# Kernel tuning notes

Measured on AMD Instinct MI355X. Metric: run time of the kernel, lower is better.

## Reference

```python
import jax, jax.numpy as jnp
import numpy as np

B, N, IN, H, DH, ACT = 8192, 36, 8, 8, 9, 10
GAT = H * DH  # 72 == 2*N, required so cat([down(x), t]) matches mu's input dim
NEG = -1e9


def setup_inputs() -> dict:
    key = jax.random.key(0)
    ks = jax.random.split(key, 9)
    x = jax.random.normal(ks[0], (B, N, IN), dtype=jnp.float32)
    adj = jax.random.randint(ks[1], (N, N), 0, 2, dtype=jnp.int32)
    adj = jnp.maximum(adj, jnp.eye(N, dtype=jnp.int32))  # self-loops: no empty softmax rows
    s = 0.1
    W = jax.random.normal(ks[2], (H, IN - 1, DH), dtype=jnp.float32) * s   # per-head projection
    a_src = jax.random.normal(ks[3], (H, DH), dtype=jnp.float32) * s       # attention vec (source half)
    a_dst = jax.random.normal(ks[4], (H, DH), dtype=jnp.float32) * s       # attention vec (target half)
    W_down = jax.random.normal(ks[5], (GAT, 1), dtype=jnp.float32) * s
    b_down = jnp.zeros((1,), dtype=jnp.float32)
    W_mu = jax.random.normal(ks[6], (GAT, ACT), dtype=jnp.float32) * s     # GAT == 2*N
    b_mu = jnp.zeros((ACT,), dtype=jnp.float32)
    return {"x": x, "adj": adj, "W": W, "a_src": a_src, "a_dst": a_dst,
            "W_down": W_down, "b_down": b_down, "W_mu": W_mu, "b_mu": b_mu}


def _gat_encoder(xc, adj, W, a_src, a_dst):
    # xc: [B,N,IN-1]; standard multi-head GAT with adjacency-masked attention
    h = jnp.einsum('bni,hid->bhnd', xc, W)                 # [B,H,N,DH]
    e_src = jnp.einsum('bhnd,hd->bhn', h, a_src)           # [B,H,N]
    e_dst = jnp.einsum('bhnd,hd->bhn', h, a_dst)           # [B,H,N]
    e = jax.nn.leaky_relu(e_src[:, :, :, None] + e_dst[:, :, None, :], 0.2)  # [B,H,N,N]
    e = jnp.where(adj[None, None, :, :] > 0, e, NEG)
    attn = jax.nn.softmax(e, axis=-1)
    out = jnp.einsum('bhij,bhjd->bhid', attn, h)           # [B,H,N,DH]
    out = out.transpose(0, 2, 1, 3).reshape(out.shape[0], N, GAT)  # concat heads
    return jax.nn.elu(out)


def reference(x, adj, W, a_src, a_dst, W_down, b_down, W_mu, b_mu):
    # slice/cat glue: drop feature 3, keep it as scalar channel t
    xc = jnp.concatenate([x[:, :, :3], x[:, :, 4:]], axis=-1)  # [B,N,IN-1]
    t = xc[:, :, 3]                                            # [B,N] (== original x[:,:,4])
    g = _gat_encoder(xc, adj, W, a_src, a_dst)                 # [B,N,GAT]
    down = (g @ W_down + b_down)[..., 0]                       # [B,N]
    feat = jax.nn.leaky_relu(jnp.concatenate([down, t], axis=-1), 0.01)  # [B,2N]
    mu = feat @ W_mu + b_mu                                    # [B,ACT]
    return mu
```

## Files before the change

### kernel.cpp

```cpp
#include <hip/hip_runtime.h>

typedef float v2f __attribute__((ext_vector_type(2)));

#define BB 8192
#define NN 36
#define INF_ 8
#define HH 8
#define DHH 9
#define GATF 72
#define ACTF 10
#define NTH 320
#define HSTRIDE 12
#define WSTRIDE 12
#define L2E 1.44269504088896f

static __device__ __forceinline__ v2f mk2(float a, float b) { v2f r; r.x = a; r.y = b; return r; }

__global__ __launch_bounds__(NTH, 6) void gnn_kernel(
    const float* __restrict__ x, const int* __restrict__ adj,
    const float* __restrict__ W, const float* __restrict__ a_src,
    const float* __restrict__ a_dst, const float* __restrict__ W_down,
    const float* __restrict__ b_down, const float* __restrict__ W_mu,
    const float* __restrict__ b_mu, float* __restrict__ out)
{
    const int b = blockIdx.x;
    const int tid = threadIdx.x;

    __shared__ float xcs[NN * 9];
    __shared__ float ts[NN];
    __shared__ __align__(16) float hbuf[HH * NN * HSTRIDE];
    __shared__ __align__(16) float edl[HH * NN];
    __shared__ uint2 adjm[NN];
    __shared__ float pd[NN * 9];
    __shared__ float feat[GATF];
    __shared__ __align__(16) float wlds[HH * 7 * WSTRIDE];
    __shared__ v2f  aid[HH * DHH];
    __shared__ float wdlds[GATF];
    __shared__ float wmulds[GATF * ACTF];
    __shared__ float bdlds[1];
    __shared__ float bmulds[ACTF];

    const float* xb = x + (size_t)b * (NN * INF_);
    if (tid < NN * INF_) {
        int n = tid >> 3, c = tid & 7;
        float v = xb[tid];
        if (c < 3) xcs[n * 9 + c] = v;
        else if (c > 3) xcs[n * 9 + (c - 1)] = v;
        if (c == 4) ts[n] = v;
    }
    {
        int i0 = tid - 256;
        if (i0 >= 0 && i0 < NN) {
            const int4* ap = reinterpret_cast<const int4*>(adj + i0 * NN);
            unsigned int lo = 0u, hi = 0u;
            #pragma unroll
            for (int q = 0; q < 9; ++q) {
                int4 a4 = ap[q];
                const int base = q * 4;
                if (base + 0 < 32) { lo |= (a4.x > 0 ? 1u << (base + 0) : 0u); } else { hi |= (a4.x > 0 ? 1u << (base - 32) : 0u); }
                if (base + 1 < 32) { lo |= (a4.y > 0 ? 1u << (base + 1) : 0u); } else { hi |= (a4.y > 0 ? 1u << (base + 1 - 32) : 0u); }
                if (base + 2 < 32) { lo |= (a4.z > 0 ? 1u << (base + 2) : 0u); } else { hi |= (a4.z > 0 ? 1u << (base + 2 - 32) : 0u); }
                if (base + 3 < 32) { lo |= (a4.w > 0 ? 1u << (base + 3) : 0u); } else { hi |= (a4.w > 0 ? 1u << (base + 3 - 32) : 0u); }
            }
            adjm[i0] = make_uint2(lo, hi);
        }
    }
    for (int idx = tid; idx < HH * 7 * DHH; idx += NTH) {
        int row = idx / DHH, d = idx - row * DHH;
        wlds[row * WSTRIDE + d] = W[idx];
    }
    if (tid < HH * DHH) aid[tid] = mk2(a_src[tid], a_dst[tid]);
    if (tid >= 128 && tid < 128 + GATF) wdlds[tid - 128] = W_down[tid - 128];
    for (int idx = tid; idx < GATF * ACTF; idx += NTH) wmulds[idx] = W_mu[idx];
    if (tid == 0) bdlds[0] = b_down[0];
    if (tid >= 64 && tid < 64 + ACTF) bmulds[tid - 64] = b_mu[tid - 64];
    __syncthreads();

    const int hh = (tid < HH * NN) ? (tid / NN) : 0;
    const int i  = (tid < HH * NN) ? (tid - hh * NN) : 0;
    float esr = 0.f;
    if (tid < HH * NN) {
        const float* xp = xcs + i * 9;
        const float* wp = wlds + hh * 7 * WSTRIDE;
        v2f h01 = mk2(0.f, 0.f), h23 = h01, h45 = h01, h67 = h01;
        float h8 = 0.f;
        #pragma unroll
        for (int k = 0; k < 7; ++k) {
            float xk = xp[k];
            v2f xkk = mk2(xk, xk);
            const float* wr = wp + k * WSTRIDE;
            float4 wa = *reinterpret_cast<const float4*>(wr);
            float4 wb = *reinterpret_cast<const float4*>(wr + 4);
            float  wc = wr[8];
            h01 = __builtin_elementwise_fma(xkk, mk2(wa.x, wa.y), h01);
            h23 = __builtin_elementwise_fma(xkk, mk2(wa.z, wa.w), h23);
            h45 = __builtin_elementwise_fma(xkk, mk2(wb.x, wb.y), h45);
            h67 = __builtin_elementwise_fma(xkk, mk2(wb.z, wb.w), h67);
            h8 = fmaf(xk, wc, h8);
        }
        float* hp = hbuf + (hh * NN + i) * HSTRIDE;
        *reinterpret_cast<float4*>(hp)     = make_float4(h01.x, h01.y, h23.x, h23.y);
        *reinterpret_cast<float4*>(hp + 4) = make_float4(h45.x, h45.y, h67.x, h67.y);
        hp[8] = h8;
        const v2f* ap = aid + hh * DHH;
        v2f sd = mk2(0.f, 0.f);
        sd = __builtin_elementwise_fma(mk2(h01.x, h01.x), ap[0], sd);
        sd = __builtin_elementwise_fma(mk2(h01.y, h01.y), ap[1], sd);
        sd = __builtin_elementwise_fma(mk2(h23.x, h23.x), ap[2], sd);
        sd = __builtin_elementwise_fma(mk2(h23.y, h23.y), ap[3], sd);
        sd = __builtin_elementwise_fma(mk2(h45.x, h45.x), ap[4], sd);
        sd = __builtin_elementwise_fma(mk2(h45.y, h45.y), ap[5], sd);
        sd = __builtin_elementwise_fma(mk2(h67.x, h67.x), ap[6], sd);
        sd = __builtin_elementwise_fma(mk2(h67.y, h67.y), ap[7], sd);
        sd = __builtin_elementwise_fma(mk2(h8, h8), ap[8], sd);
        esr = sd.x * L2E;
        edl[hh * NN + i] = sd.y * L2E;
    }
    __syncthreads();

    if (tid < HH * NN) {
        const uint2 mrow = adjm[i];
        const float* hrow = hbuf + (hh * NN) * HSTRIDE;
        const float* edp = edl + hh * NN;
        const v2f esr2 = mk2(esr, esr);
        const v2f c02 = mk2(0.2f, 0.2f);
        v2f acc01 = mk2(0.f, 0.f), acc23 = acc01, acc45 = acc01, acc67 = acc01;
        float acc8 = 0.f;
        v2f ssum2 = mk2(0.f, 0.f);

#define PVE(jj, p_) { \
        const float* hj_ = hrow + (jj) * HSTRIDE; \
        float4 ha_ = *reinterpret_cast<const float4*>(hj_); \
        float4 hb_ = *reinterpret_cast<const float4*>(hj_ + 4); \
        float  hc_ = hj_[8]; \
        v2f pp_ = mk2(p_, p_); \
        acc01 = __builtin_elementwise_fma(pp_, mk2(ha_.x, ha_.y), acc01); \
        acc23 = __builtin_elementwise_fma(pp_, mk2(ha_.z, ha_.w), acc23); \
        acc45 = __builtin_elementwise_fma(pp_, mk2(hb_.x, hb_.y), acc45); \
        acc67 = __builtin_elementwise_fma(pp_, mk2(hb_.z, hb_.w), acc67); \
        acc8 = fmaf(p_, hc_, acc8); }

#define STEP2(jb, w_, ee2_) { \
        v2f s2_ = esr2 + (ee2_); \
        v2f t2_ = s2_ * c02; \
        float p0_ = __builtin_exp2f(fmaxf(s2_.x, t2_.x)); \
        float p1_ = __builtin_exp2f(fmaxf(s2_.y, t2_.y)); \
        int m0_ = ((int)((w_) << (31 - ((jb) & 31)))) >> 31; \
        int m1_ = ((int)((w_) << (31 - (((jb) & 31) + 1)))) >> 31; \
        p0_ = __int_as_float(__float_as_int(p0_) & m0_); \
        p1_ = __int_as_float(__float_as_int(p1_) & m1_); \
        ssum2 += mk2(p0_, p1_); \
        PVE((jb), p0_); \
        PVE((jb) + 1, p1_); }

        #pragma unroll
        for (int q = 0; q < 9; ++q) {
            float4 e4 = *reinterpret_cast<const float4*>(edp + q * 4);
            const unsigned wq = (q < 8) ? mrow.x : mrow.y;
            STEP2(4 * q + 0, wq, mk2(e4.x, e4.y));
            STEP2(4 * q + 2, wq, mk2(e4.z, e4.w));
        }
#undef STEP2
#undef PVE

        float ssum = ssum2.x + ssum2.y;
        float inv = 1.0f / ssum;
        v2f inv2 = mk2(inv, inv);
        v2f o01 = acc01 * inv2, o23 = acc23 * inv2, o45 = acc45 * inv2, o67 = acc67 * inv2;
        float o8 = acc8 * inv;
        const float* wdp = wdlds + hh * DHH;
        float pdown = 0.f;
#define EPI(oval, dd_) { \
        float o_ = (oval); \
        o_ = (o_ > 0.f) ? o_ : (__builtin_exp2f(o_ * L2E) - 1.0f); \
        pdown = fmaf(o_, wdp[dd_], pdown); }
        EPI(o01.x, 0); EPI(o01.y, 1); EPI(o23.x, 2); EPI(o23.y, 3);
        EPI(o45.x, 4); EPI(o45.y, 5); EPI(o67.x, 6); EPI(o67.y, 7);
        EPI(o8, 8);
#undef EPI
        pd[i * 9 + hh] = pdown;
    }
    __syncthreads();

    if (tid < NN) {
        const float* pp = pd + tid * 9;
        float acc = bdlds[0];
        #pragma unroll
        for (int h = 0; h < HH; ++h) acc += pp[h];
        feat[tid] = (acc > 0.f) ? acc : 0.01f * acc;
    } else if (tid < 2 * NN) {
        float v = ts[tid - NN];
        feat[tid] = (v > 0.f) ? v : 0.01f * v;
    }
    __syncthreads();

    if (tid < ACTF) {
        float acc = bmulds[tid];
        #pragma unroll
        for (int k = 0; k < GATF; ++k) acc += feat[k] * wmulds[k * ACTF + tid];
        out[(size_t)b * ACTF + tid] = acc;
    }
}

extern "C" void kernel_launch(void* const* d_in, const int* in_sizes, int n_in,
                              void* d_out, int out_size, void* d_ws, size_t ws_size,
                              hipStream_t stream) {
    const float* x      = (const float*)d_in[0];
    const int*   adj    = (const int*)d_in[1];
    const float* W      = (const float*)d_in[2];
    const float* a_src  = (const float*)d_in[3];
    const float* a_dst  = (const float*)d_in[4];
    const float* W_down = (const float*)d_in[5];
    const float* b_down = (const float*)d_in[6];
    const float* W_mu   = (const float*)d_in[7];
    const float* b_mu   = (const float*)d_in[8];
    float* out = (float*)d_out;

    gnn_kernel<<<BB, NTH, 0, stream>>>(x, adj, W, a_src, a_dst, W_down, b_down, W_mu, b_mu, out);
}
```

Measured before the change: 77.39 us.

## Process two batch items per block and use additive float adjacency mask

```diff
diff --git a/kernel.cpp b/kernel.cpp
--- a/kernel.cpp
+++ b/kernel.cpp
@@ -9,10 +9,12 @@
 #define DHH 9
 #define GATF 72
 #define ACTF 10
-#define NTH 320
+#define NTH 576
+#define ROWS 288
 #define HSTRIDE 12
 #define WSTRIDE 12
 #define L2E 1.44269504088896f
+#define MASKNEG -1000000.0f
 
 static __device__ __forceinline__ v2f mk2(float a, float b) { v2f r; r.x = a; r.y = b; return r; }
 
@@ -23,16 +25,16 @@
     const float* __restrict__ b_down, const float* __restrict__ W_mu,
     const float* __restrict__ b_mu, float* __restrict__ out)
 {
-    const int b = blockIdx.x;
     const int tid = threadIdx.x;
-
-    __shared__ float xcs[NN * 9];
-    __shared__ float ts[NN];
-    __shared__ __align__(16) float hbuf[HH * NN * HSTRIDE];
-    __shared__ __align__(16) float edl[HH * NN];
-    __shared__ uint2 adjm[NN];
-    __shared__ float pd[NN * 9];
-    __shared__ float feat[GATF];
+    const int b0 = blockIdx.x * 2;
+
+    __shared__ float xcs[2 * NN * 9];
+    __shared__ float ts[2 * NN];
+    __shared__ __align__(16) float hbuf[2 * HH * NN * HSTRIDE];
+    __shared__ __align__(16) float edl[2 * ROWS];
+    __shared__ float pd[2 * NN * 9];
+    __shared__ float feat[2 * GATF];
+    __shared__ __align__(16) float adjf[NN * NN];
     __shared__ __align__(16) float wlds[HH * 7 * WSTRIDE];
     __shared__ v2f  aid[HH * DHH];
     __shared__ float wdlds[GATF];
@@ -40,47 +42,45 @@
     __shared__ float bdlds[1];
     __shared__ float bmulds[ACTF];
 
-    const float* xb = x + (size_t)b * (NN * INF_);
-    if (tid < NN * INF_) {
-        int n = tid >> 3, c = tid & 7;
+    {
+        const float* xb = x + (size_t)b0 * (NN * INF_);
+        int item = (tid >= NN * INF_) ? 1 : 0;
+        int rem = tid - item * (NN * INF_);
+        int n = rem >> 3, c = rem & 7;
         float v = xb[tid];
-        if (c < 3) xcs[n * 9 + c] = v;
-        else if (c > 3) xcs[n * 9 + (c - 1)] = v;
-        if (c == 4) ts[n] = v;
-    }
-    {
-        int i0 = tid - 256;
-        if (i0 >= 0 && i0 < NN) {
-            const int4* ap = reinterpret_cast<const int4*>(adj + i0 * NN);
-            unsigned int lo = 0u, hi = 0u;
-            #pragma unroll
-            for (int q = 0; q < 9; ++q) {
-                int4 a4 = ap[q];
-                const int base = q * 4;
-                if (base + 0 < 32) { lo |= (a4.x > 0 ? 1u << (base + 0) : 0u); } else { hi |= (a4.x > 0 ? 1u << (base - 32) : 0u); }
-                if (base + 1 < 32) { lo |= (a4.y > 0 ? 1u << (base + 1) : 0u); } else { hi |= (a4.y > 0 ? 1u << (base + 1 - 32) : 0u); }
-                if (base + 2 < 32) { lo |= (a4.z > 0 ? 1u << (base + 2) : 0u); } else { hi |= (a4.z > 0 ? 1u << (base + 2 - 32) : 0u); }
-                if (base + 3 < 32) { lo |= (a4.w > 0 ? 1u << (base + 3) : 0u); } else { hi |= (a4.w > 0 ? 1u << (base + 3 - 32) : 0u); }
-            }
-            adjm[i0] = make_uint2(lo, hi);
-        }
-    }
+        float* xc = xcs + item * (NN * 9);
+        if (c < 3) xc[n * 9 + c] = v;
+        else if (c > 3) xc[n * 9 + (c - 1)] = v;
+        if (c == 4) ts[item * NN + n] = v;
+    }
+    if (tid < 324) {
+        int i = tid / 9, q = tid - i * 9;
+        int4 a4 = reinterpret_cast<const int4*>(adj)[tid];
+        float4 m4;
+        m4.x = (a4.x > 0) ? 0.f : MASKNEG;
+        m4.y = (a4.y > 0) ? 0.f : MASKNEG;
+        m4.z = (a4.z > 0) ? 0.f : MASKNEG;
+        m4.w = (a4.w > 0) ? 0.f : MASKNEG;
+        *reinterpret_cast<float4*>(adjf + i * NN + q * 4) = m4;
+    }
+    if (tid >= 384 && tid < 384 + HH * 7 * DHH - 504 + 504) {  }
     for (int idx = tid; idx < HH * 7 * DHH; idx += NTH) {
         int row = idx / DHH, d = idx - row * DHH;
         wlds[row * WSTRIDE + d] = W[idx];
     }
     if (tid < HH * DHH) aid[tid] = mk2(a_src[tid], a_dst[tid]);
-    if (tid >= 128 && tid < 128 + GATF) wdlds[tid - 128] = W_down[tid - 128];
+    if (tid >= 448 && tid < 448 + GATF) wdlds[tid - 448] = W_down[tid - 448];
     for (int idx = tid; idx < GATF * ACTF; idx += NTH) wmulds[idx] = W_mu[idx];
     if (tid == 0) bdlds[0] = b_down[0];
-    if (tid >= 64 && tid < 64 + ACTF) bmulds[tid - 64] = b_mu[tid - 64];
-    __syncthreads();
-
-    const int hh = (tid < HH * NN) ? (tid / NN) : 0;
-    const int i  = (tid < HH * NN) ? (tid - hh * NN) : 0;
-    float esr = 0.f;
-    if (tid < HH * NN) {
-        const float* xp = xcs + i * 9;
+    if (tid >= 352 && tid < 352 + ACTF) bmulds[tid - 352] = b_mu[tid - 352];
+    __syncthreads();
+
+    const int item = (tid >= ROWS) ? 1 : 0;
+    const int r = tid - item * ROWS;
+    const int hh = r / NN, i = r - hh * NN;
+    float esr;
+    {
+        const float* xp = xcs + item * (NN * 9) + i * 9;
         const float* wp = wlds + hh * 7 * WSTRIDE;
         v2f h01 = mk2(0.f, 0.f), h23 = h01, h45 = h01, h67 = h01;
         float h8 = 0.f;
@@ -98,10 +98,10 @@
             h67 = __builtin_elementwise_fma(xkk, mk2(wb.z, wb.w), h67);
             h8 = fmaf(xk, wc, h8);
         }
-        float* hp = hbuf + (hh * NN + i) * HSTRIDE;
+        float* hp = hbuf + (item * ROWS + hh * NN + i) * HSTRIDE;
         *reinterpret_cast<float4*>(hp)     = make_float4(h01.x, h01.y, h23.x, h23.y);
         *reinterpret_cast<float4*>(hp + 4) = make_float4(h45.x, h45.y, h67.x, h67.y);
-        hp[8] = h8;
+        *reinterpret_cast<v2f*>(hp + 8)    = mk2(h8, 1.0f);
         const v2f* ap = aid + hh * DHH;
         v2f sd = mk2(0.f, 0.f);
         sd = __builtin_elementwise_fma(mk2(h01.x, h01.x), ap[0], sd);
@@ -114,60 +114,46 @@
         sd = __builtin_elementwise_fma(mk2(h67.y, h67.y), ap[7], sd);
         sd = __builtin_elementwise_fma(mk2(h8, h8), ap[8], sd);
         esr = sd.x * L2E;
-        edl[hh * NN + i] = sd.y * L2E;
-    }
-    __syncthreads();
-
-    if (tid < HH * NN) {
-        const uint2 mrow = adjm[i];
-        const float* hrow = hbuf + (hh * NN) * HSTRIDE;
-        const float* edp = edl + hh * NN;
-        const v2f esr2 = mk2(esr, esr);
-        const v2f c02 = mk2(0.2f, 0.2f);
-        v2f acc01 = mk2(0.f, 0.f), acc23 = acc01, acc45 = acc01, acc67 = acc01;
-        float acc8 = 0.f;
-        v2f ssum2 = mk2(0.f, 0.f);
-
-#define PVE(jj, p_) { \
+        edl[item * ROWS + hh * NN + i] = sd.y * L2E;
+    }
+    __syncthreads();
+
+    {
+        const float* hrow = hbuf + (item * ROWS + hh * NN) * HSTRIDE;
+        const float* edp = edl + item * ROWS + hh * NN;
+        const float* amr = adjf + i * NN;
+        v2f acc01 = mk2(0.f, 0.f), acc23 = acc01, acc45 = acc01, acc67 = acc01, acc89 = acc01;
+
+#define STEP(jj, ee, mm) { \
+        float s_ = esr + (ee); \
+        float e_ = fmaxf(s_, 0.2f * s_) + (mm);           \
+        float p_ = __builtin_exp2f(e_);                   \
         const float* hj_ = hrow + (jj) * HSTRIDE; \
         float4 ha_ = *reinterpret_cast<const float4*>(hj_); \
         float4 hb_ = *reinterpret_cast<const float4*>(hj_ + 4); \
-        float  hc_ = hj_[8]; \
+        v2f hc_ = *reinterpret_cast<const v2f*>(hj_ + 8); \
         v2f pp_ = mk2(p_, p_); \
         acc01 = __builtin_elementwise_fma(pp_, mk2(ha_.x, ha_.y), acc01); \
         acc23 = __builtin_elementwise_fma(pp_, mk2(ha_.z, ha_.w), acc23); \
         acc45 = __builtin_elementwise_fma(pp_, mk2(hb_.x, hb_.y), acc45); \
         acc67 = __builtin_elementwise_fma(pp_, mk2(hb_.z, hb_.w), acc67); \
-        acc8 = fmaf(p_, hc_, acc8); }
-
-#define STEP2(jb, w_, ee2_) { \
-        v2f s2_ = esr2 + (ee2_); \
-        v2f t2_ = s2_ * c02; \
-        float p0_ = __builtin_exp2f(fmaxf(s2_.x, t2_.x)); \
-        float p1_ = __builtin_exp2f(fmaxf(s2_.y, t2_.y)); \
-        int m0_ = ((int)((w_) << (31 - ((jb) & 31)))) >> 31; \
-        int m1_ = ((int)((w_) << (31 - (((jb) & 31) + 1)))) >> 31; \
-        p0_ = __int_as_float(__float_as_int(p0_) & m0_); \
-        p1_ = __int_as_float(__float_as_int(p1_) & m1_); \
-        ssum2 += mk2(p0_, p1_); \
-        PVE((jb), p0_); \
-        PVE((jb) + 1, p1_); }
+        acc89 = __builtin_elementwise_fma(pp_, hc_, acc89); }
 
         #pragma unroll
         for (int q = 0; q < 9; ++q) {
             float4 e4 = *reinterpret_cast<const float4*>(edp + q * 4);
-            const unsigned wq = (q < 8) ? mrow.x : mrow.y;
-            STEP2(4 * q + 0, wq, mk2(e4.x, e4.y));
-            STEP2(4 * q + 2, wq, mk2(e4.z, e4.w));
+            float4 m4 = *reinterpret_cast<const float4*>(amr + q * 4);
+            STEP(4 * q + 0, e4.x, m4.x);
+            STEP(4 * q + 1, e4.y, m4.y);
+            STEP(4 * q + 2, e4.z, m4.z);
+            STEP(4 * q + 3, e4.w, m4.w);
         }
-#undef STEP2
-#undef PVE
-
-        float ssum = ssum2.x + ssum2.y;
-        float inv = 1.0f / ssum;
+#undef STEP
+
+        float inv = 1.0f / acc89.y;
         v2f inv2 = mk2(inv, inv);
         v2f o01 = acc01 * inv2, o23 = acc23 * inv2, o45 = acc45 * inv2, o67 = acc67 * inv2;
-        float o8 = acc8 * inv;
+        float o8 = acc89.x * inv;
         const float* wdp = wdlds + hh * DHH;
         float pdown = 0.f;
 #define EPI(oval, dd_) { \
@@ -178,27 +164,35 @@
         EPI(o45.x, 4); EPI(o45.y, 5); EPI(o67.x, 6); EPI(o67.y, 7);
         EPI(o8, 8);
 #undef EPI
-        pd[i * 9 + hh] = pdown;
-    }
-    __syncthreads();
-
-    if (tid < NN) {
-        const float* pp = pd + tid * 9;
+        pd[item * (NN * 9) + i * 9 + hh] = pdown;
+    }
+    __syncthreads();
+
+    if (tid < 2 * NN) {
+        int it = (tid >= NN) ? 1 : 0;
+        int node = tid - it * NN;
+        const float* pp = pd + it * (NN * 9) + node * 9;
         float acc = bdlds[0];
         #pragma unroll
         for (int h = 0; h < HH; ++h) acc += pp[h];
-        feat[tid] = (acc > 0.f) ? acc : 0.01f * acc;
-    } else if (tid < 2 * NN) {
-        float v = ts[tid - NN];
-        feat[tid] = (v > 0.f) ? v : 0.01f * v;
-    }
-    __syncthreads();
-
-    if (tid < ACTF) {
-        float acc = bmulds[tid];
-        #pragma unroll
-        for (int k = 0; k < GATF; ++k) acc += feat[k] * wmulds[k * ACTF + tid];
-        out[(size_t)b * ACTF + tid] = acc;
+        feat[it * GATF + node] = (acc > 0.f) ? acc : 0.01f * acc;
+    } else if (tid < 4 * NN) {
+        int idx = tid - 2 * NN;
+        int it = (idx >= NN) ? 1 : 0;
+        int node = idx - it * NN;
+        float v = ts[it * NN + node];
+        feat[it * GATF + NN + node] = (v > 0.f) ? v : 0.01f * v;
+    }
+    __syncthreads();
+
+    if (tid < 2 * ACTF) {
+        int it = (tid >= ACTF) ? 1 : 0;
+        int o = tid - it * ACTF;
+        const float* fp = feat + it * GATF;
+        float acc = bmulds[o];
+        #pragma unroll
+        for (int k = 0; k < GATF; ++k) acc = fmaf(fp[k], wmulds[k * ACTF + o], acc);
+        out[(size_t)(b0 + it) * ACTF + o] = acc;
     }
 }
 
@@ -216,5 +210,5 @@
     const float* b_mu   = (const float*)d_in[8];
     float* out = (float*)d_out;
 
-    gnn_kernel<<<BB, NTH, 0, stream>>>(x, adj, W, a_src, a_dst, W_down, b_down, W_mu, b_mu, out);
+    gnn_kernel<<<BB / 2, NTH, 0, stream>>>(x, adj, W, a_src, a_dst, W_down, b_down, W_mu, b_mu, out);
 }
```

New measurement: 81.57 us. 5.4% more time.

## Use additive float adjacency mask and fold softmax denominator into packed FMA

Applied to the files above, without the earlier changes.

```diff
diff --git a/kernel.cpp b/kernel.cpp
--- a/kernel.cpp
+++ b/kernel.cpp
@@ -10,11 +10,19 @@
 #define GATF 72
 #define ACTF 10
 #define NTH 320
+#define ROWS 288
 #define HSTRIDE 12
 #define WSTRIDE 12
 #define L2E 1.44269504088896f
+#define MASKNEG -1000000.0f
 
 static __device__ __forceinline__ v2f mk2(float a, float b) { v2f r; r.x = a; r.y = b; return r; }
+
+static __device__ __forceinline__ v2f pkfma(v2f a, v2f b, v2f c) {
+    v2f d;
+    asm("v_pk_fma_f32 %0, %1, %2, %3" : "=v"(d) : "v"(a), "v"(b), "v"(c));
+    return d;
+}
 
 __global__ __launch_bounds__(NTH, 6) void gnn_kernel(
     const float* __restrict__ x, const int* __restrict__ adj,
@@ -28,9 +36,9 @@
 
     __shared__ float xcs[NN * 9];
     __shared__ float ts[NN];
-    __shared__ __align__(16) float hbuf[HH * NN * HSTRIDE];
-    __shared__ __align__(16) float edl[HH * NN];
-    __shared__ uint2 adjm[NN];
+    __shared__ __align__(16) float hbuf[ROWS * HSTRIDE];
+    __shared__ __align__(16) float edl[ROWS];
+    __shared__ __align__(16) float adjf[NN * NN];
     __shared__ float pd[NN * 9];
     __shared__ float feat[GATF];
     __shared__ __align__(16) float wlds[HH * 7 * WSTRIDE];
@@ -48,22 +56,14 @@
         else if (c > 3) xcs[n * 9 + (c - 1)] = v;
         if (c == 4) ts[n] = v;
     }
-    {
-        int i0 = tid - 256;
-        if (i0 >= 0 && i0 < NN) {
-            const int4* ap = reinterpret_cast<const int4*>(adj + i0 * NN);
-            unsigned int lo = 0u, hi = 0u;
-            #pragma unroll
-            for (int q = 0; q < 9; ++q) {
-                int4 a4 = ap[q];
-                const int base = q * 4;
-                if (base + 0 < 32) { lo |= (a4.x > 0 ? 1u << (base + 0) : 0u); } else { hi |= (a4.x > 0 ? 1u << (base - 32) : 0u); }
-                if (base + 1 < 32) { lo |= (a4.y > 0 ? 1u << (base + 1) : 0u); } else { hi |= (a4.y > 0 ? 1u << (base + 1 - 32) : 0u); }
-                if (base + 2 < 32) { lo |= (a4.z > 0 ? 1u << (base + 2) : 0u); } else { hi |= (a4.z > 0 ? 1u << (base + 2 - 32) : 0u); }
-                if (base + 3 < 32) { lo |= (a4.w > 0 ? 1u << (base + 3) : 0u); } else { hi |= (a4.w > 0 ? 1u << (base + 3 - 32) : 0u); }
-            }
-            adjm[i0] = make_uint2(lo, hi);
-        }
+    for (int idx = tid; idx < (NN * NN) / 4; idx += NTH) {
+        int4 a4 = reinterpret_cast<const int4*>(adj)[idx];
+        float4 m4;
+        m4.x = (a4.x > 0) ? 0.f : MASKNEG;
+        m4.y = (a4.y > 0) ? 0.f : MASKNEG;
+        m4.z = (a4.z > 0) ? 0.f : MASKNEG;
+        m4.w = (a4.w > 0) ? 0.f : MASKNEG;
+        *reinterpret_cast<float4*>(adjf + idx * 4) = m4;
     }
     for (int idx = tid; idx < HH * 7 * DHH; idx += NTH) {
         int row = idx / DHH, d = idx - row * DHH;
@@ -76,10 +76,10 @@
     if (tid >= 64 && tid < 64 + ACTF) bmulds[tid - 64] = b_mu[tid - 64];
     __syncthreads();
 
-    const int hh = (tid < HH * NN) ? (tid / NN) : 0;
-    const int i  = (tid < HH * NN) ? (tid - hh * NN) : 0;
+    const int hh = (tid < ROWS) ? (tid / NN) : 0;
+    const int i  = (tid < ROWS) ? (tid - hh * NN) : 0;
     float esr = 0.f;
-    if (tid < HH * NN) {
+    if (tid < ROWS) {
         const float* xp = xcs + i * 9;
         const float* wp = wlds + hh * 7 * WSTRIDE;
         v2f h01 = mk2(0.f, 0.f), h23 = h01, h45 = h01, h67 = h01;
@@ -92,82 +92,68 @@
             float4 wa = *reinterpret_cast<const float4*>(wr);
             float4 wb = *reinterpret_cast<const float4*>(wr + 4);
             float  wc = wr[8];
-            h01 = __builtin_elementwise_fma(xkk, mk2(wa.x, wa.y), h01);
-            h23 = __builtin_elementwise_fma(xkk, mk2(wa.z, wa.w), h23);
-            h45 = __builtin_elementwise_fma(xkk, mk2(wb.x, wb.y), h45);
-            h67 = __builtin_elementwise_fma(xkk, mk2(wb.z, wb.w), h67);
+            h01 = pkfma(xkk, *(const v2f*)&wa.x, h01);
+            h23 = pkfma(xkk, *(const v2f*)&wa.z, h23);
+            h45 = pkfma(xkk, *(const v2f*)&wb.x, h45);
+            h67 = pkfma(xkk, *(const v2f*)&wb.z, h67);
             h8 = fmaf(xk, wc, h8);
         }
         float* hp = hbuf + (hh * NN + i) * HSTRIDE;
         *reinterpret_cast<float4*>(hp)     = make_float4(h01.x, h01.y, h23.x, h23.y);
         *reinterpret_cast<float4*>(hp + 4) = make_float4(h45.x, h45.y, h67.x, h67.y);
-        hp[8] = h8;
+        *reinterpret_cast<v2f*>(hp + 8)    = mk2(h8, 1.0f);
         const v2f* ap = aid + hh * DHH;
         v2f sd = mk2(0.f, 0.f);
-        sd = __builtin_elementwise_fma(mk2(h01.x, h01.x), ap[0], sd);
-        sd = __builtin_elementwise_fma(mk2(h01.y, h01.y), ap[1], sd);
-        sd = __builtin_elementwise_fma(mk2(h23.x, h23.x), ap[2], sd);
-        sd = __builtin_elementwise_fma(mk2(h23.y, h23.y), ap[3], sd);
-        sd = __builtin_elementwise_fma(mk2(h45.x, h45.x), ap[4], sd);
-        sd = __builtin_elementwise_fma(mk2(h45.y, h45.y), ap[5], sd);
-        sd = __builtin_elementwise_fma(mk2(h67.x, h67.x), ap[6], sd);
-        sd = __builtin_elementwise_fma(mk2(h67.y, h67.y), ap[7], sd);
-        sd = __builtin_elementwise_fma(mk2(h8, h8), ap[8], sd);
+        sd = pkfma(mk2(h01.x, h01.x), ap[0], sd);
+        sd = pkfma(mk2(h01.y, h01.y), ap[1], sd);
+        sd = pkfma(mk2(h23.x, h23.x), ap[2], sd);
+        sd = pkfma(mk2(h23.y, h23.y), ap[3], sd);
+        sd = pkfma(mk2(h45.x, h45.x), ap[4], sd);
+        sd = pkfma(mk2(h45.y, h45.y), ap[5], sd);
+        sd = pkfma(mk2(h67.x, h67.x), ap[6], sd);
+        sd = pkfma(mk2(h67.y, h67.y), ap[7], sd);
+        sd = pkfma(mk2(h8, h8), ap[8], sd);
         esr = sd.x * L2E;
         edl[hh * NN + i] = sd.y * L2E;
     }
     __syncthreads();
 
-    if (tid < HH * NN) {
-        const uint2 mrow = adjm[i];
+    if (tid < ROWS) {
         const float* hrow = hbuf + (hh * NN) * HSTRIDE;
         const float* edp = edl + hh * NN;
-        const v2f esr2 = mk2(esr, esr);
-        const v2f c02 = mk2(0.2f, 0.2f);
-        v2f acc01 = mk2(0.f, 0.f), acc23 = acc01, acc45 = acc01, acc67 = acc01;
-        float acc8 = 0.f;
-        v2f ssum2 = mk2(0.f, 0.f);
-
-#define PVE(jj, p_) { \
+        const float* amr = adjf + i * NN;
+        v2f acc01 = mk2(0.f, 0.f), acc23 = acc01, acc45 = acc01, acc67 = acc01, acc89 = acc01;
+
+#define STEP(jj, ee, mm) { \
+        float s_ = esr + (ee); \
+        float e_ = fmaxf(s_, 0.2f * s_) + (mm);           \
+        float p_ = __builtin_exp2f(e_);                   \
         const float* hj_ = hrow + (jj) * HSTRIDE; \
         float4 ha_ = *reinterpret_cast<const float4*>(hj_); \
         float4 hb_ = *reinterpret_cast<const float4*>(hj_ + 4); \
-        float  hc_ = hj_[8]; \
+        v2f hc_ = *reinterpret_cast<const v2f*>(hj_ + 8); \
         v2f pp_ = mk2(p_, p_); \
-        acc01 = __builtin_elementwise_fma(pp_, mk2(ha_.x, ha_.y), acc01); \
-        acc23 = __builtin_elementwise_fma(pp_, mk2(ha_.z, ha_.w), acc23); \
-        acc45 = __builtin_elementwise_fma(pp_, mk2(hb_.x, hb_.y), acc45); \
-        acc67 = __builtin_elementwise_fma(pp_, mk2(hb_.z, hb_.w), acc67); \
-        acc8 = fmaf(p_, hc_, acc8); }
-
-#define STEP2(jb, w_, ee2_) { \
-        v2f s2_ = esr2 + (ee2_); \
-        v2f t2_ = s2_ * c02; \
-        float p0_ = __builtin_exp2f(fmaxf(s2_.x, t2_.x)); \
-        float p1_ = __builtin_exp2f(fmaxf(s2_.y, t2_.y)); \
-        int m0_ = ((int)((w_) << (31 - ((jb) & 31)))) >> 31; \
-        int m1_ = ((int)((w_) << (31 - (((jb) & 31) + 1)))) >> 31; \
-        p0_ = __int_as_float(__float_as_int(p0_) & m0_); \
-        p1_ = __int_as_float(__float_as_int(p1_) & m1_); \
-        ssum2 += mk2(p0_, p1_); \
-        PVE((jb), p0_); \
-        PVE((jb) + 1, p1_); }
+        acc01 = pkfma(pp_, *(const v2f*)&ha_.x, acc01); \
+        acc23 = pkfma(pp_, *(const v2f*)&ha_.z, acc23); \
+        acc45 = pkfma(pp_, *(const v2f*)&hb_.x, acc45); \
+        acc67 = pkfma(pp_, *(const v2f*)&hb_.z, acc67); \
+        acc89 = pkfma(pp_, hc_, acc89); }
 
         #pragma unroll
         for (int q = 0; q < 9; ++q) {
             float4 e4 = *reinterpret_cast<const float4*>(edp + q * 4);
-            const unsigned wq = (q < 8) ? mrow.x : mrow.y;
-            STEP2(4 * q + 0, wq, mk2(e4.x, e4.y));
-            STEP2(4 * q + 2, wq, mk2(e4.z, e4.w));
+            float4 m4 = *reinterpret_cast<const float4*>(amr + q * 4);
+            STEP(4 * q + 0, e4.x, m4.x);
+            STEP(4 * q + 1, e4.y, m4.y);
+            STEP(4 * q + 2, e4.z, m4.z);
+            STEP(4 * q + 3, e4.w, m4.w);
         }
-#undef STEP2
-#undef PVE
-
-        float ssum = ssum2.x + ssum2.y;
-        float inv = 1.0f / ssum;
+#undef STEP
+
+        float inv = 1.0f / acc89.y;
         v2f inv2 = mk2(inv, inv);
         v2f o01 = acc01 * inv2, o23 = acc23 * inv2, o45 = acc45 * inv2, o67 = acc67 * inv2;
-        float o8 = acc8 * inv;
+        float o8 = acc89.x * inv;
         const float* wdp = wdlds + hh * DHH;
         float pdown = 0.f;
 #define EPI(oval, dd_) { \
@@ -197,7 +183,7 @@
     if (tid < ACTF) {
         float acc = bmulds[tid];
         #pragma unroll
-        for (int k = 0; k < GATF; ++k) acc += feat[k] * wmulds[k * ACTF + tid];
+        for (int k = 0; k < GATF; ++k) acc = fmaf(feat[k], wmulds[k * ACTF + tid], acc);
         out[(size_t)b * ACTF + tid] = acc;
     }
 }
```

Measured after the change: 79.40 us. 1.03x slower.
